# Optimization experiments

Hardware: AMD Instinct MI355X
Metric: run time of the kernel (lower is better)

## Reference

```python
import jax, jax.numpy as jnp
import numpy as np

B, S, D, F, H, E = 2, 1024, 1024, 4096, 16, 8
EPS = 1e-5


def _layernorm(x, w, b):
    m = jnp.mean(x, -1, keepdims=True)
    v = jnp.var(x, -1, keepdims=True)
    return (x - m) * jax.lax.rsqrt(v + EPS) * w + b


def _rope(x):
    # rotary embedding applied over full embed dim (split-half convention)
    b, s, d = x.shape
    half = d // 2
    inv = 1.0 / (10000.0 ** (jnp.arange(half, dtype=jnp.float32) / half))
    ang = jnp.arange(s, dtype=jnp.float32)[:, None] * inv[None, :]  # [S, half]
    cos, sin = jnp.cos(ang), jnp.sin(ang)
    x1, x2 = x[..., :half], x[..., half:]
    return jnp.concatenate([x1 * cos - x2 * sin, x1 * sin + x2 * cos], -1)


def setup_inputs() -> dict:
    key = jax.random.key(0)
    ks = jax.random.split(key, 9)
    sc = 0.02
    return {
        "x": jax.random.normal(ks[0], (B, S, D), jnp.float32),
        "ln1_w": jnp.ones((D,), jnp.float32),
        "ln1_b": jnp.zeros((D,), jnp.float32),
        "ln2_w": jnp.ones((D,), jnp.float32),
        "ln2_b": jnp.zeros((D,), jnp.float32),
        "w_qkv": jax.random.normal(ks[1], (3 * D, D), jnp.float32) * sc,
        "b_qkv": jnp.zeros((3 * D,), jnp.float32),
        "w_out": jax.random.normal(ks[2], (D, D), jnp.float32) * sc,
        "b_out": jnp.zeros((D,), jnp.float32),
        "w_router": jax.random.normal(ks[3], (D, E), jnp.float32) * sc,
        "wi": jax.random.normal(ks[4], (E, D, F), jnp.float32) * sc,  # per-expert wi (no bias)
        "wo": jax.random.normal(ks[5], (E, F // 2, D), jnp.float32) * sc,  # swiglu halves ffn dim
    }


def reference(x, ln1_w, ln1_b, ln2_w, ln2_b, w_qkv, b_qkv, w_out, b_out, w_router, wi, wo):
    # ---- pre-norm self-attention block ----
    residual = x
    h = _layernorm(x, ln1_w, ln1_b)
    h = _rope(h)
    qkv = h @ w_qkv.T + b_qkv  # [B,S,3D]
    q, k, v = jnp.split(qkv, 3, axis=-1)
    hd = D // H
    to_heads = lambda t: t.reshape(B, S, H, hd).transpose(0, 2, 1, 3)
    q, k, v = to_heads(q), to_heads(k), to_heads(v)
    scale = 1.0 / np.sqrt(hd).astype(np.float32)
    att = jax.nn.softmax(jnp.einsum('bhqd,bhkd->bhqk', q, k) * scale, axis=-1)
    o = jnp.einsum('bhqk,bhkd->bhqd', att, v).transpose(0, 2, 1, 3).reshape(B, S, D)
    o = o @ w_out.T + b_out
    x = residual + o  # attn dropout is identity at eval

    # ---- pre-norm sparse MoE FFN block ----
    residual = x
    h = _layernorm(x, ln2_w, ln2_b)
    # top-1 router in float32
    logits = h.astype(jnp.float32) @ w_router  # [B,S,E]
    probs = jax.nn.softmax(logits, axis=-1)
    mask = jax.nn.one_hot(jnp.argmax(probs, -1), E, dtype=h.dtype)  # expert_mask
    gate = probs.astype(h.dtype) * mask  # router_probs * expert_mask, [B,S,E]
    # dense all-expert compute, masked combine (same math as gather/scatter loop)
    hid = jnp.einsum('bsd,edf->bsef', h, wi)  # [B,S,E,F]
    a, g = jnp.split(hid, 2, axis=-1)
    act = jax.nn.silu(a) * g  # SwiGLU, [B,S,E,F/2]
    y = jnp.einsum('bsef,efd,bse->bsd', act, wo, gate)
    x = residual + y
    return x, logits
```

## Files before the change

### kernel.cpp

```cpp
#include <hip/hip_runtime.h>
#include <hip/hip_bf16.h>
#include <math.h>

#define BB 2
#define SS 1024
#define DD 1024
#define FF 4096
#define HH 16
#define EE 8
#define MM (BB*SS)
#define MAX_TILES 24
#define MAX_TILES2 40

typedef __attribute__((ext_vector_type(8))) short bf16x8;
typedef __attribute__((ext_vector_type(8))) short s16x8;
typedef __attribute__((ext_vector_type(4))) float f32x4;

#define OFF_WIT  ((size_t)0)
#define OFF_WOT  ((size_t)67108864)
#define OFF_WQH  ((size_t)100663296)
#define OFF_WQL  ((size_t)106954752)
#define OFF_WOH  ((size_t)113246208)
#define OFF_WOL  ((size_t)115343360)
#define OFF_H1H  ((size_t)117440512)
#define OFF_H1L  ((size_t)121634816)
#define OFF_QKV  ((size_t)125829120)
#define OFF_OH   ((size_t)150994944)
#define OFF_OL   ((size_t)155189248)
#define OFF_X2   ((size_t)159383552)
#define OFF_H2B  ((size_t)167772160)
#define OFF_ACT  ((size_t)171966464)
#define OFF_GATE ((size_t)180879360)
#define OFF_EID  ((size_t)180887552)
#define OFF_PERM ((size_t)180895744)
#define OFF_CNT  ((size_t)180903936)
#define OFF_FILL ((size_t)180903968)
#define OFF_NT   ((size_t)180904000)
#define OFF_TE   ((size_t)180904192)
#define OFF_TS   ((size_t)180904320)
#define OFF_TR   ((size_t)180904448)
#define OFF_TE2  ((size_t)180904576)
#define OFF_TS2  ((size_t)180904768)
#define OFF_TR2  ((size_t)180904960)
#define OFF_NT2  ((size_t)180905152)
#define OFF_KSH  OFF_WQH
#define OFF_KSL  (OFF_WQH + 4194304)
#define OFF_VTH  OFF_H1H
#define OFF_VTL  OFF_H1L

__device__ __forceinline__ void gload16(const void* g, void* l) {
    __builtin_amdgcn_global_load_lds(
        (const __attribute__((address_space(1))) unsigned int*)g,
        (__attribute__((address_space(3))) unsigned int*)l, 16, 0, 0);
}

__device__ __forceinline__ short bfh(float v) {
    __hip_bfloat16 h = __float2bfloat16(v);
    return *(short*)&h;
}
__device__ __forceinline__ float bf2f(short s) {
    __hip_bfloat16 h = *(__hip_bfloat16*)&s;
    return __bfloat162float(h);
}

__device__ __forceinline__ void split_write(float v, __hip_bfloat16* hp, __hip_bfloat16* lp, size_t idx) {
    __hip_bfloat16 h = __float2bfloat16(v);
    hp[idx] = h;
    lp[idx] = __float2bfloat16(v - __bfloat162float(h));
}

__device__ __forceinline__ void tcvt64_body(const float* __restrict__ in, __hip_bfloat16* __restrict__ out,
                                            int R, int C, int r0, int c0, float* tile , int t) {
    {
        int ri = t >> 2, cj = (t & 3) * 16;
        const float* ip = &in[(size_t)(r0 + ri) * C + c0 + cj];
#pragma unroll
        for (int k = 0; k < 4; ++k) {
            float4 v = *(const float4*)(ip + k * 4);
            tile[ri * 65 + cj + k * 4 + 0] = v.x;
            tile[ri * 65 + cj + k * 4 + 1] = v.y;
            tile[ri * 65 + cj + k * 4 + 2] = v.z;
            tile[ri * 65 + cj + k * 4 + 3] = v.w;
        }
    }
    __syncthreads();
    {
        int co = t >> 2, rj = (t & 3) * 16;
        bf16x8 v8a, v8b;
#pragma unroll
        for (int q = 0; q < 8; ++q) v8a[q] = bfh(tile[(rj + q) * 65 + co]);
#pragma unroll
        for (int q = 0; q < 8; ++q) v8b[q] = bfh(tile[(rj + 8 + q) * 65 + co]);
        __hip_bfloat16* op = &out[(size_t)(c0 + co) * R + r0 + rj];
        *(bf16x8*)op = v8a;
        *(bf16x8*)(op + 8) = v8b;
    }
}

__global__ void k_phase0(const float* __restrict__ x, const float* __restrict__ ln1w,
                         const float* __restrict__ ln1b,
                         __hip_bfloat16* __restrict__ h1H, __hip_bfloat16* __restrict__ h1L,
                         const float* __restrict__ w_qkv, __hip_bfloat16* __restrict__ wqH,
                         __hip_bfloat16* __restrict__ wqL,
                         const float* __restrict__ w_out, __hip_bfloat16* __restrict__ woH,
                         __hip_bfloat16* __restrict__ woL) {
    __shared__ __align__(16) float smem[1032];
    int bid = blockIdx.x, t = threadIdx.x;
    if (bid < 2048) {
        int m = bid, s = m & (SS - 1);
        float* row = smem;
        float* red = smem + 1024;
        const float* xp = x + (size_t)m * DD;
        float sum = 0.f, sumsq = 0.f;
#pragma unroll
        for (int l = 0; l < 4; ++l) {
            int i = t + l * 256;
            float v = xp[i];
            row[i] = v;
            sum += v; sumsq += v * v;
        }
#pragma unroll
        for (int off = 32; off; off >>= 1) {
            sum   += __shfl_xor(sum, off);
            sumsq += __shfl_xor(sumsq, off);
        }
        int wid = t >> 6, lane = t & 63;
        if (lane == 0) { red[wid] = sum; red[4 + wid] = sumsq; }
        __syncthreads();
        sum   = red[0] + red[1] + red[2] + red[3];
        sumsq = red[4] + red[5] + red[6] + red[7];
        float mean = sum * (1.f / DD);
        float var  = sumsq * (1.f / DD) - mean * mean;
        float rstd = rsqrtf(var + 1e-5f);
        size_t base = (size_t)m * DD;
        const float kln = logf(10000.f) / 512.f;
#pragma unroll
        for (int l = 0; l < 2; ++l) {
            int i = t + l * 256;
            float n1 = (row[i]       - mean) * rstd * ln1w[i]       + ln1b[i];
            float n2 = (row[i + 512] - mean) * rstd * ln1w[i + 512] + ln1b[i + 512];
            float inv = expf(-(float)i * kln);
            float ang = (float)s * inv;
            float c = cosf(ang), sn = sinf(ang);
            split_write(n1 * c - n2 * sn,  h1H, h1L, base + i);
            split_write(n1 * sn + n2 * c, h1H, h1L, base + i + 512);
        }
    } else if (bid < 5120) {
        int idx = (bid - 2048) * 256 + t;
        float4 v = ((const float4*)w_qkv)[idx];
        split_write(v.x, wqH, wqL, (size_t)idx * 4 + 0);
        split_write(v.y, wqH, wqL, (size_t)idx * 4 + 1);
        split_write(v.z, wqH, wqL, (size_t)idx * 4 + 2);
        split_write(v.w, wqH, wqL, (size_t)idx * 4 + 3);
    } else {
        int idx = (bid - 5120) * 256 + t;
        float4 v = ((const float4*)w_out)[idx];
        split_write(v.x, woH, woL, (size_t)idx * 4 + 0);
        split_write(v.y, woH, woL, (size_t)idx * 4 + 1);
        split_write(v.z, woH, woL, (size_t)idx * 4 + 2);
        split_write(v.w, woH, woL, (size_t)idx * 4 + 3);
    }
}

__global__ void k_qkv(const __hip_bfloat16* __restrict__ Ah, const __hip_bfloat16* __restrict__ Al,
                      const __hip_bfloat16* __restrict__ Bh, const __hip_bfloat16* __restrict__ Bl,
                      const float* __restrict__ bias, float* __restrict__ Cf) {
    __shared__ __align__(16) short AsH[64 * 32];
    __shared__ __align__(16) short AsL[64 * 32];
    __shared__ __align__(16) short BsH[128 * 32];
    __shared__ __align__(16) short BsL[128 * 32];
    const int N = 3072, K = DD;
    int bid = blockIdx.x;
    int xcd = bid & 7, idx = bid >> 3;
    int nt = xcd + (idx >> 5) * 8;
    int mt = idx & 31;
    int m0 = mt * 64, n0 = nt * 128;
    const int t = threadIdx.x;
    const int w = t >> 6, lane = t & 63;
    const int sid = w * 64 + lane;
    const int g = lane >> 4, r16 = lane & 15;

    f32x4 acc[4][2] = {};

    for (int k0 = 0; k0 < K; k0 += 32) {
        {
            int rrow = sid >> 2, sl = sid & 3;
            int slog = sl ^ ((rrow >> 1) & 3);
            size_t lbase = (size_t)(w * 64) * 8;
            size_t gaoff = (size_t)(m0 + rrow) * K + k0 + slog * 8;
            gload16(Ah + gaoff, &AsH[lbase]);
            gload16(Al + gaoff, &AsL[lbase]);
        }
#pragma unroll
        for (int j = 0; j < 2; ++j) {
            int id = j * 256 + sid;
            int rrow = id >> 2, sl = id & 3;
            int slog = sl ^ ((rrow >> 1) & 3);
            size_t lbase = (size_t)(j * 256 + w * 64) * 8;
            size_t gboff = (size_t)(n0 + rrow) * K + k0 + slog * 8;
            gload16(Bh + gboff, &BsH[lbase]);
            gload16(Bl + gboff, &BsL[lbase]);
        }
        __syncthreads();
        bf16x8 ah[4], al[4], bh[2], bl[2];
#pragma unroll
        for (int i = 0; i < 4; ++i) {
            int ra = i * 16 + r16;
            int pa = g ^ ((ra >> 1) & 3);
            ah[i] = *(const bf16x8*)&AsH[ra * 32 + pa * 8];
            al[i] = *(const bf16x8*)&AsL[ra * 32 + pa * 8];
        }
#pragma unroll
        for (int n = 0; n < 2; ++n) {
            int rb = w * 32 + n * 16 + r16;
            int pb = g ^ ((rb >> 1) & 3);
            bh[n] = *(const bf16x8*)&BsH[rb * 32 + pb * 8];
            bl[n] = *(const bf16x8*)&BsL[rb * 32 + pb * 8];
        }
#pragma unroll
        for (int i = 0; i < 4; ++i)
#pragma unroll
            for (int n = 0; n < 2; ++n) {
                acc[i][n] = __builtin_amdgcn_mfma_f32_16x16x32_bf16(ah[i], bh[n], acc[i][n], 0, 0, 0);
                acc[i][n] = __builtin_amdgcn_mfma_f32_16x16x32_bf16(ah[i], bl[n], acc[i][n], 0, 0, 0);
                acc[i][n] = __builtin_amdgcn_mfma_f32_16x16x32_bf16(al[i], bh[n], acc[i][n], 0, 0, 0);
            }
        __syncthreads();
    }

#pragma unroll
    for (int i = 0; i < 4; ++i) {
#pragma unroll
        for (int n = 0; n < 2; ++n) {
            int col = n0 + w * 32 + n * 16 + r16;
#pragma unroll
            for (int q = 0; q < 4; ++q) {
                int r = m0 + i * 16 + g * 4 + q;
                Cf[(size_t)r * N + col] = acc[i][n][q] + bias[col];
            }
        }
    }
}

__global__ void k_oproj64(const __hip_bfloat16* __restrict__ Ah, const __hip_bfloat16* __restrict__ Al,
                          const __hip_bfloat16* __restrict__ Bh, const __hip_bfloat16* __restrict__ Bl,
                          const float* __restrict__ bias, const float* __restrict__ addsrc,
                          float* __restrict__ Cf, int* __restrict__ zero17) {
    __shared__ __align__(16) short AsH[64 * 32];
    __shared__ __align__(16) short AsL[64 * 32];
    __shared__ __align__(16) short BsH[128 * 32];
    __shared__ __align__(16) short BsL[128 * 32];
    const int N = DD, K = DD;
    int bid = blockIdx.x;
    int m0 = (bid >> 3) * 64, n0 = (bid & 7) * 128;
    const int t = threadIdx.x;
    if (bid == 0 && t < 17) zero17[t] = 0;
    const int w = t >> 6, lane = t & 63;
    const int sid = w * 64 + lane;
    const int g = lane >> 4, r16 = lane & 15;

    f32x4 acc[4][2] = {};

    for (int k0 = 0; k0 < K; k0 += 32) {
        {
            int rrow = sid >> 2, sl = sid & 3;
            int slog = sl ^ ((rrow >> 1) & 3);
            size_t lbase = (size_t)(w * 64) * 8;
            size_t gaoff = (size_t)(m0 + rrow) * K + k0 + slog * 8;
            gload16(Ah + gaoff, &AsH[lbase]);
            gload16(Al + gaoff, &AsL[lbase]);
        }
#pragma unroll
        for (int j = 0; j < 2; ++j) {
            int id = j * 256 + sid;
            int rrow = id >> 2, sl = id & 3;
            int slog = sl ^ ((rrow >> 1) & 3);
            size_t lbase = (size_t)(j * 256 + w * 64) * 8;
            size_t gboff = (size_t)(n0 + rrow) * K + k0 + slog * 8;
            gload16(Bh + gboff, &BsH[lbase]);
            gload16(Bl + gboff, &BsL[lbase]);
        }
        __syncthreads();
        bf16x8 ah[4], al[4], bh[2], bl[2];
#pragma unroll
        for (int i = 0; i < 4; ++i) {
            int ra = i * 16 + r16;
            int pa = g ^ ((ra >> 1) & 3);
            ah[i] = *(const bf16x8*)&AsH[ra * 32 + pa * 8];
            al[i] = *(const bf16x8*)&AsL[ra * 32 + pa * 8];
        }
#pragma unroll
        for (int n = 0; n < 2; ++n) {
            int rb = w * 32 + n * 16 + r16;
            int pb = g ^ ((rb >> 1) & 3);
            bh[n] = *(const bf16x8*)&BsH[rb * 32 + pb * 8];
            bl[n] = *(const bf16x8*)&BsL[rb * 32 + pb * 8];
        }
#pragma unroll
        for (int i = 0; i < 4; ++i)
#pragma unroll
            for (int n = 0; n < 2; ++n) {
                acc[i][n] = __builtin_amdgcn_mfma_f32_16x16x32_bf16(ah[i], bh[n], acc[i][n], 0, 0, 0);
                acc[i][n] = __builtin_amdgcn_mfma_f32_16x16x32_bf16(ah[i], bl[n], acc[i][n], 0, 0, 0);
                acc[i][n] = __builtin_amdgcn_mfma_f32_16x16x32_bf16(al[i], bh[n], acc[i][n], 0, 0, 0);
            }
        __syncthreads();
    }

#pragma unroll
    for (int i = 0; i < 4; ++i) {
#pragma unroll
        for (int n = 0; n < 2; ++n) {
            int col = n0 + w * 32 + n * 16 + r16;
#pragma unroll
            for (int q = 0; q < 4; ++q) {
                int r = m0 + i * 16 + g * 4 + q;
                Cf[(size_t)r * N + col] =
                    acc[i][n][q] + bias[col] + addsrc[(size_t)r * N + col];
            }
        }
    }
}

__global__ void k_moe_up(const __hip_bfloat16* __restrict__ A,
                         const __hip_bfloat16* __restrict__ Bt,
                         __hip_bfloat16* __restrict__ act,
                         const int* __restrict__ perm,
                         const int* __restrict__ te, const int* __restrict__ ts,
                         const int* __restrict__ tr, const int* __restrict__ ntl) {
    __shared__ __align__(16) short As[128 * 32];
    __shared__ __align__(16) short Bs[128 * 32];
    __shared__ int permS[128];
    int tile = blockIdx.y;
    if (tile >= *ntl) return;
    int e = te[tile], rs = ts[tile], rows = tr[tile];
    const int t = threadIdx.x;
    if (t < 128) permS[t] = (t < rows) ? perm[rs + t] : 0;
    __syncthreads();
    int c0 = blockIdx.x * 64;
    const int w = t >> 6, lane = t & 63;
    const int wr = w >> 1, wc = w & 1;
    const int sid = w * 64 + lane;
    const int g = lane >> 4, r16 = lane & 15;

    const __hip_bfloat16* Bp = Bt + (size_t)e * FF * DD;

    f32x4 acc[4][4] = {};

    for (int k0 = 0; k0 < DD; k0 += 32) {
#pragma unroll
        for (int j = 0; j < 2; ++j) {
            int id = j * 256 + sid;
            int rrow = id >> 2, sl = id & 3;
            int slog = sl ^ ((rrow >> 1) & 3);
            size_t lbase = (size_t)(j * 256 + w * 64) * 8;
            gload16(A + (size_t)permS[rrow] * DD + k0 + slog * 8, &As[lbase]);
            int q = rrow >> 4, rr = rrow & 15;
            int wrow = c0 + (q >> 2) * 32 + ((q & 3) >> 1) * 16 + rr + (q & 1) * 2048;
            gload16(Bp + (size_t)wrow * DD + k0 + slog * 8, &Bs[lbase]);
        }
        __syncthreads();
        bf16x8 af[4], bfr[4];
#pragma unroll
        for (int i = 0; i < 4; ++i) {
            int ra = wr * 64 + i * 16 + r16;
            int pa = g ^ ((ra >> 1) & 3);
            af[i] = *(const bf16x8*)&As[ra * 32 + pa * 8];
            int rb = wc * 64 + i * 16 + r16;
            int pb = g ^ ((rb >> 1) & 3);
            bfr[i] = *(const bf16x8*)&Bs[rb * 32 + pb * 8];
        }
#pragma unroll
        for (int i = 0; i < 4; ++i)
#pragma unroll
            for (int n = 0; n < 4; ++n)
                acc[i][n] = __builtin_amdgcn_mfma_f32_16x16x32_bf16(af[i], bfr[n], acc[i][n], 0, 0, 0);
        __syncthreads();
    }

#pragma unroll
    for (int i = 0; i < 4; ++i) {
#pragma unroll
        for (int p2 = 0; p2 < 2; ++p2) {
            int col = c0 + wc * 32 + p2 * 16 + r16;
#pragma unroll
            for (int q = 0; q < 4; ++q) {
                int r = wr * 64 + i * 16 + g * 4 + q;
                if (r < rows) {
                    float a  = acc[i][2 * p2][q];
                    float gv = acc[i][2 * p2 + 1][q];
                    act[(size_t)(rs + r) * 2048 + col] =
                        __float2bfloat16((a / (1.f + expf(-a))) * gv);
                }
            }
        }
    }
}

__global__ void k_moe_dn(const __hip_bfloat16* __restrict__ A,
                         const __hip_bfloat16* __restrict__ Bt,
                         const float* __restrict__ addsrc, float* __restrict__ Cf,
                         const int* __restrict__ perm,
                         const int* __restrict__ te2, const int* __restrict__ ts2,
                         const int* __restrict__ tr2, const int* __restrict__ ntl2,
                         const float* __restrict__ gate) {
    __shared__ __align__(16) short As[64 * 32];
    __shared__ __align__(16) short Bs[128 * 32];
    __shared__ int permS[64];
    int tile = blockIdx.y;
    if (tile >= *ntl2) return;
    int e = te2[tile], rs = ts2[tile], rows = tr2[tile];
    const int t = threadIdx.x;
    if (t < 64) permS[t] = (t < rows) ? perm[rs + t] : 0;
    __syncthreads();
    int n0 = blockIdx.x * 128;
    const int w = t >> 6, lane = t & 63;
    const int sid = w * 64 + lane;
    const int g = lane >> 4, r16 = lane & 15;
    const int K = FF / 2;

    const __hip_bfloat16* Bp = Bt + (size_t)e * DD * (FF / 2);

    f32x4 acc[4][2] = {};

    for (int k0 = 0; k0 < K; k0 += 32) {
        {
            int rrow = sid >> 2, sl = sid & 3;
            int slog = sl ^ ((rrow >> 1) & 3);
            size_t lbase = (size_t)(w * 64) * 8;
            gload16(A + (size_t)(rs + rrow) * K + k0 + slog * 8, &As[lbase]);
        }
#pragma unroll
        for (int j = 0; j < 2; ++j) {
            int id = j * 256 + sid;
            int rrow = id >> 2, sl = id & 3;
            int slog = sl ^ ((rrow >> 1) & 3);
            size_t lbase = (size_t)(j * 256 + w * 64) * 8;
            gload16(Bp + (size_t)(n0 + rrow) * K + k0 + slog * 8, &Bs[lbase]);
        }
        __syncthreads();
        bf16x8 af[4], bfr[2];
#pragma unroll
        for (int i = 0; i < 4; ++i) {
            int ra = i * 16 + r16;
            int pa = g ^ ((ra >> 1) & 3);
            af[i] = *(const bf16x8*)&As[ra * 32 + pa * 8];
        }
#pragma unroll
        for (int n = 0; n < 2; ++n) {
            int rb = w * 32 + n * 16 + r16;
            int pb = g ^ ((rb >> 1) & 3);
            bfr[n] = *(const bf16x8*)&Bs[rb * 32 + pb * 8];
        }
#pragma unroll
        for (int i = 0; i < 4; ++i)
#pragma unroll
            for (int n = 0; n < 2; ++n)
                acc[i][n] = __builtin_amdgcn_mfma_f32_16x16x32_bf16(af[i], bfr[n], acc[i][n], 0, 0, 0);
        __syncthreads();
    }

#pragma unroll
    for (int i = 0; i < 4; ++i) {
#pragma unroll
        for (int n = 0; n < 2; ++n) {
            int col = n0 + w * 32 + n * 16 + r16;
#pragma unroll
            for (int q = 0; q < 4; ++q) {
                int r = i * 16 + g * 4 + q;
                if (r >= rows) continue;
                int tok = permS[r];
                Cf[(size_t)tok * DD + col] = addsrc[(size_t)tok * DD + col] + gate[tok] * acc[i][n][q];
            }
        }
    }
}

__global__ void k_prep(const float* __restrict__ qkv, short* __restrict__ KH, short* __restrict__ KL,
                       short* __restrict__ VH, short* __restrict__ VL) {
    __shared__ float tile[64][65];
    int b = blockIdx.z, h = blockIdx.y, s0 = blockIdx.x * 64;
    int t = threadIdx.x;
    int row = t >> 2, c0 = (t & 3) * 16;
    const float* kp = qkv + (size_t)(b * SS + s0 + row) * 3072 + 1024 + h * 64 + c0;
    const float* vp = kp + 1024;
    {
        size_t krow = ((size_t)(b * HH + h) * SS + s0 + row) * 64;
        int key = (s0 + row) & 7;
#pragma unroll
        for (int g2 = 0; g2 < 2; ++g2) {
            s16x8 hv, lv;
#pragma unroll
            for (int j = 0; j < 8; ++j) {
                float v = kp[g2 * 8 + j];
                short hh = bfh(v);
                hv[j] = hh; lv[j] = bfh(v - bf2f(hh));
            }
            int p = ((c0 >> 3) + g2) ^ key;
            *(s16x8*)&KH[krow + p * 8] = hv;
            *(s16x8*)&KL[krow + p * 8] = lv;
        }
    }
#pragma unroll
    for (int j = 0; j < 16; ++j) tile[row][c0 + j] = vp[j];
    __syncthreads();
    {
        int d = t >> 2, sc = (t & 3) * 16;
        size_t vrow = ((size_t)(b * HH + h) * 64 + d) * SS + s0;
        int key = d & 7;
#pragma unroll
        for (int g2 = 0; g2 < 2; ++g2) {
            s16x8 hv, lv;
#pragma unroll
            for (int j = 0; j < 8; ++j) {
                float v = tile[sc + g2 * 8 + j][d];
                short hh = bfh(v);
                hv[j] = hh; lv[j] = bfh(v - bf2f(hh));
            }
            int p = ((sc >> 3) + g2) ^ key;
            *(s16x8*)&VH[vrow + p * 8] = hv;
            *(s16x8*)&VL[vrow + p * 8] = lv;
        }
    }
}

#define LDP 72
__global__ __launch_bounds__(512, 4)
void k_attn_mega(const float* __restrict__ qkv,
                 const short* __restrict__ KH, const short* __restrict__ KL,
                 const short* __restrict__ VH, const short* __restrict__ VL,
                 __hip_bfloat16* __restrict__ ohi, __hip_bfloat16* __restrict__ olo,
                 const float* __restrict__ wi, __hip_bfloat16* __restrict__ wiT,
                 const float* __restrict__ wo, __hip_bfloat16* __restrict__ woT) {
    __shared__ __align__(16) char smem[69632];
    int id = blockIdx.x;
    if (id >= 256) {
        int t512 = threadIdx.x;
        int half = t512 >> 8, t = t512 & 255;
        float* tile = (float*)(smem + half * 33280 / 2 * 2);
        tile = (float*)(smem + half * 16640);
        if (id < 4352) {
            int gidx = (id - 256) * 2 + half;
            int e = gidx >> 10, rem = gidx & 1023;
            int ry = rem >> 6, cx = rem & 63;
            tcvt64_body(wi + (size_t)e * DD * FF, wiT + (size_t)e * DD * FF,
                        1024, 4096, ry * 64, cx * 64, tile, t);
        } else {
            int gidx = (id - 4352) * 2 + half;
            int e = gidx >> 9, rem = gidx & 511;
            int ry = rem >> 4, cx = rem & 15;
            tcvt64_body(wo + (size_t)e * 2048 * 1024, woT + (size_t)e * 2048 * 1024,
                        2048, 1024, ry * 64, cx * 64, tile, t);
        }
        return;
    }
    short* Ks  = (short*)smem;
    short* Kl2 = (short*)(smem + 8192);
    short* Vs  = (short*)(smem + 16384);
    short* Vl2 = (short*)(smem + 24576);
    int xcd = id & 7, slot = id >> 3;
    int bh = xcd * 4 + (slot >> 3);
    int q0 = (slot & 7) * 128;
    int b = bh >> 4, h = bh & 15;
    int t = threadIdx.x;
    int w = t >> 6, lane = t & 63;
    int g = lane >> 4, r16 = lane & 15;
    int srow = t >> 3, sslot = t & 7;
    short* PhS = (short*)(smem + 32768 + w * 2304);
    short* PlS = (short*)(smem + 51200 + w * 2304);

    const size_t kbase = ((size_t)bh * SS) * 64;
    const size_t vbase = ((size_t)bh * 64) * SS;

    bf16x8 qfh[2], qfl[2];
    {
        const float* qp = qkv + (size_t)(b * SS + q0 + w * 16 + r16) * 3072 + h * 64;
#pragma unroll
        for (int ks = 0; ks < 2; ++ks) {
            float vv[8];
            *(float4*)&vv[0] = *(const float4*)(qp + ks * 32 + g * 8);
            *(float4*)&vv[4] = *(const float4*)(qp + ks * 32 + g * 8 + 4);
#pragma unroll
            for (int j = 0; j < 8; ++j) {
                float sv = vv[j] * 0.125f;
                short hh = bfh(sv);
                qfh[ks][j] = hh;
                qfl[ks][j] = bfh(sv - bf2f(hh));
            }
        }
    }

    float mrun[4], lrun[4];
    f32x4 oacc[4] = {};
#pragma unroll
    for (int q = 0; q < 4; ++q) { mrun[q] = -1e30f; lrun[q] = 0.f; }

    for (int k0 = 0; k0 < SS; k0 += 64) {
        gload16(KH + kbase + (size_t)(k0 + srow) * 64 + sslot * 8, Ks  + w * 512);
        gload16(KL + kbase + (size_t)(k0 + srow) * 64 + sslot * 8, Kl2 + w * 512);
        gload16(VH + vbase + (size_t)srow * SS + k0 + sslot * 8,   Vs  + w * 512);
        gload16(VL + vbase + (size_t)srow * SS + k0 + sslot * 8,   Vl2 + w * 512);
        __syncthreads();

        f32x4 accs[4] = {};
#pragma unroll
        for (int ks = 0; ks < 2; ++ks) {
            bf16x8 kfh[4], kfl[4];
#pragma unroll
            for (int n = 0; n < 4; ++n) {
                int rb = n * 16 + r16;
                int p = (ks * 4 + g) ^ (r16 & 7);
                kfh[n] = *(const bf16x8*)&Ks[rb * 64 + p * 8];
                kfl[n] = *(const bf16x8*)&Kl2[rb * 64 + p * 8];
            }
            __builtin_amdgcn_s_setprio(1);
#pragma unroll
            for (int n = 0; n < 4; ++n) {
                accs[n] = __builtin_amdgcn_mfma_f32_16x16x32_bf16(qfh[ks], kfh[n], accs[n], 0, 0, 0);
                accs[n] = __builtin_amdgcn_mfma_f32_16x16x32_bf16(qfh[ks], kfl[n], accs[n], 0, 0, 0);
                accs[n] = __builtin_amdgcn_mfma_f32_16x16x32_bf16(qfl[ks], kfh[n], accs[n], 0, 0, 0);
            }
            __builtin_amdgcn_s_setprio(0);
        }

        float mn[4], corr[4], psum[4];
#pragma unroll
        for (int q = 0; q < 4; ++q) {
            float m = fmaxf(fmaxf(accs[0][q], accs[1][q]), fmaxf(accs[2][q], accs[3][q]));
            m = fmaxf(m, __shfl_xor(m, 1));
            m = fmaxf(m, __shfl_xor(m, 2));
            m = fmaxf(m, __shfl_xor(m, 4));
            m = fmaxf(m, __shfl_xor(m, 8));
            mn[q] = fmaxf(mrun[q], m);
            corr[q] = expf(mrun[q] - mn[q]);
            mrun[q] = mn[q];
            psum[q] = 0.f;
        }
#pragma unroll
        for (int n = 0; n < 4; ++n)
#pragma unroll
            for (int q = 0; q < 4; ++q) {
                float p = expf(accs[n][q] - mn[q]);
                psum[q] += p;
                short ph = bfh(p);
                PhS[(g * 4 + q) * LDP + n * 16 + r16] = ph;
                PlS[(g * 4 + q) * LDP + n * 16 + r16] = bfh(p - bf2f(ph));
            }
#pragma unroll
        for (int q = 0; q < 4; ++q) {
            psum[q] += __shfl_xor(psum[q], 1);
            psum[q] += __shfl_xor(psum[q], 2);
            psum[q] += __shfl_xor(psum[q], 4);
            psum[q] += __shfl_xor(psum[q], 8);
            lrun[q] = lrun[q] * corr[q] + psum[q];
#pragma unroll
            for (int n = 0; n < 4; ++n) oacc[n][q] *= corr[q];
        }

#pragma unroll
        for (int ks = 0; ks < 2; ++ks) {
            bf16x8 vfh[4], vfl[4];
#pragma unroll
            for (int n = 0; n < 4; ++n) {
                int rb = n * 16 + r16;
                int p = (ks * 4 + g) ^ (r16 & 7);
                vfh[n] = *(const bf16x8*)&Vs[rb * 64 + p * 8];
                vfl[n] = *(const bf16x8*)&Vl2[rb * 64 + p * 8];
            }
            bf16x8 pfh = *(const bf16x8*)&PhS[r16 * LDP + ks * 32 + g * 8];
            bf16x8 pfl = *(const bf16x8*)&PlS[r16 * LDP + ks * 32 + g * 8];
            __builtin_amdgcn_s_setprio(1);
#pragma unroll
            for (int n = 0; n < 4; ++n) {
                oacc[n] = __builtin_amdgcn_mfma_f32_16x16x32_bf16(pfh, vfh[n], oacc[n], 0, 0, 0);
                oacc[n] = __builtin_amdgcn_mfma_f32_16x16x32_bf16(pfh, vfl[n], oacc[n], 0, 0, 0);
                oacc[n] = __builtin_amdgcn_mfma_f32_16x16x32_bf16(pfl, vfh[n], oacc[n], 0, 0, 0);
            }
            __builtin_amdgcn_s_setprio(0);
        }
        __syncthreads();
    }

    float invl[4];
#pragma unroll
    for (int q = 0; q < 4; ++q) invl[q] = 1.f / lrun[q];
#pragma unroll
    for (int n = 0; n < 4; ++n) {
        int col = h * 64 + n * 16 + r16;
#pragma unroll
        for (int q = 0; q < 4; ++q) {
            int rowg = b * SS + q0 + w * 16 + g * 4 + q;
            split_write(oacc[n][q] * invl[q], ohi, olo, (size_t)rowg * DD + col);
        }
    }
}

__global__ void k_ln2_router(const float* __restrict__ x2, const float* __restrict__ w,
                             const float* __restrict__ b, const float* __restrict__ wr,
                             __hip_bfloat16* __restrict__ h2b, float* __restrict__ logits,
                             float* __restrict__ gate, int* __restrict__ eid,
                             int* __restrict__ counts) {
    int m = blockIdx.x, t = threadIdx.x;
    __shared__ float red[8];
    __shared__ float racc[4][8];
    const float* xp = x2 + (size_t)m * DD;
    float v[4];
    float sum = 0.f, sumsq = 0.f;
#pragma unroll
    for (int l = 0; l < 4; ++l) {
        v[l] = xp[t + l * 256];
        sum += v[l]; sumsq += v[l] * v[l];
    }
#pragma unroll
    for (int off = 32; off; off >>= 1) {
        sum   += __shfl_xor(sum, off);
        sumsq += __shfl_xor(sumsq, off);
    }
    int wid = t >> 6, lane = t & 63;
    if (lane == 0) { red[wid] = sum; red[4 + wid] = sumsq; }
    __syncthreads();
    sum   = red[0] + red[1] + red[2] + red[3];
    sumsq = red[4] + red[5] + red[6] + red[7];
    float mean = sum * (1.f / DD);
    float var  = sumsq * (1.f / DD) - mean * mean;
    float rstd = rsqrtf(var + 1e-5f);
    float acc[EE] = {};
#pragma unroll
    for (int l = 0; l < 4; ++l) {
        int i = t + l * 256;
        float hv = (v[l] - mean) * rstd * w[i] + b[i];
        h2b[(size_t)m * DD + i] = __float2bfloat16(hv);
        const float* wp = wr + (size_t)i * EE;
#pragma unroll
        for (int n = 0; n < EE; ++n) acc[n] += hv * wp[n];
    }
#pragma unroll
    for (int off = 32; off; off >>= 1)
#pragma unroll
        for (int n = 0; n < EE; ++n) acc[n] += __shfl_xor(acc[n], off);
    if (lane == 0)
#pragma unroll
        for (int n = 0; n < EE; ++n) racc[wid][n] = acc[n];
    __syncthreads();
    if (t == 0) {
        float lg[EE];
#pragma unroll
        for (int n = 0; n < EE; ++n) lg[n] = racc[0][n] + racc[1][n] + racc[2][n] + racc[3][n];
        float mx = lg[0]; int best = 0;
#pragma unroll
        for (int n = 1; n < EE; ++n) if (lg[n] > mx) { mx = lg[n]; best = n; }
        float den = 0.f;
#pragma unroll
        for (int n = 0; n < EE; ++n) den += expf(lg[n] - mx);
        gate[m] = 1.f / den;
        eid[m] = best;
        atomicAdd(&counts[best], 1);
#pragma unroll
        for (int n = 0; n < EE; ++n) logits[(size_t)m * EE + n] = lg[n];
    }
}

__global__ void k_offscatter(const int* __restrict__ counts,
                             int* __restrict__ te, int* __restrict__ ts, int* __restrict__ tr,
                             int* __restrict__ ntl,
                             int* __restrict__ te2, int* __restrict__ ts2, int* __restrict__ tr2,
                             int* __restrict__ ntl2,
                             const int* __restrict__ eid,
                             int* __restrict__ fill, int* __restrict__ perm) {
    __shared__ int soffs[EE];
    int t = threadIdx.x;
    if (t == 0) {
        int off = 0, nt = 0, nt2 = 0;
        for (int e = 0; e < EE; ++e) {
            soffs[e] = off;
            int c = counts[e];
            for (int t0 = 0; t0 < c; t0 += 128) {
                te[nt] = e; ts[nt] = off + t0; tr[nt] = (c - t0 < 128) ? (c - t0) : 128; ++nt;
            }
            for (int t0 = 0; t0 < c; t0 += 64) {
                te2[nt2] = e; ts2[nt2] = off + t0; tr2[nt2] = (c - t0 < 64) ? (c - t0) : 64; ++nt2;
            }
            off += c;
        }
        *ntl = nt;
        *ntl2 = nt2;
    }
    __syncthreads();
#pragma unroll
    for (int tok = t; tok < MM; tok += 1024) {
        int e = eid[tok];
        int pos = soffs[e] + atomicAdd(&fill[e], 1);
        perm[pos] = tok;
    }
}

extern "C" void kernel_launch(void* const* d_in, const int* in_sizes, int n_in,
                              void* d_out, int out_size, void* d_ws, size_t ws_size,
                              hipStream_t stream) {
    const float* x     = (const float*)d_in[0];
    const float* ln1w  = (const float*)d_in[1];
    const float* ln1b  = (const float*)d_in[2];
    const float* ln2w  = (const float*)d_in[3];
    const float* ln2b  = (const float*)d_in[4];
    const float* w_qkv = (const float*)d_in[5];
    const float* b_qkv = (const float*)d_in[6];
    const float* w_out = (const float*)d_in[7];
    const float* b_out = (const float*)d_in[8];
    const float* w_rtr = (const float*)d_in[9];
    const float* wi    = (const float*)d_in[10];
    const float* wo    = (const float*)d_in[11];
    float* out = (float*)d_out;

    char* wsb = (char*)d_ws;
    __hip_bfloat16* wiT  = (__hip_bfloat16*)(wsb + OFF_WIT);
    __hip_bfloat16* woT  = (__hip_bfloat16*)(wsb + OFF_WOT);
    __hip_bfloat16* wqH  = (__hip_bfloat16*)(wsb + OFF_WQH);
    __hip_bfloat16* wqL  = (__hip_bfloat16*)(wsb + OFF_WQL);
    __hip_bfloat16* woH  = (__hip_bfloat16*)(wsb + OFF_WOH);
    __hip_bfloat16* woL  = (__hip_bfloat16*)(wsb + OFF_WOL);
    __hip_bfloat16* h1H  = (__hip_bfloat16*)(wsb + OFF_H1H);
    __hip_bfloat16* h1L  = (__hip_bfloat16*)(wsb + OFF_H1L);
    float*          qkvF = (float*)(wsb + OFF_QKV);
    __hip_bfloat16* oH   = (__hip_bfloat16*)(wsb + OFF_OH);
    __hip_bfloat16* oL   = (__hip_bfloat16*)(wsb + OFF_OL);
    float*          x2F  = (float*)(wsb + OFF_X2);
    __hip_bfloat16* h2B  = (__hip_bfloat16*)(wsb + OFF_H2B);
    __hip_bfloat16* actB = (__hip_bfloat16*)(wsb + OFF_ACT);
    short* KSH = (short*)(wsb + OFF_KSH);
    short* KSL = (short*)(wsb + OFF_KSL);
    short* VTH = (short*)(wsb + OFF_VTH);
    short* VTL = (short*)(wsb + OFF_VTL);
    float* gate = (float*)(wsb + OFF_GATE);
    int* eid    = (int*)(wsb + OFF_EID);
    int* perm   = (int*)(wsb + OFF_PERM);
    int* counts = (int*)(wsb + OFF_CNT);
    int* fill   = (int*)(wsb + OFF_FILL);
    int* ntl    = (int*)(wsb + OFF_NT);
    int* te     = (int*)(wsb + OFF_TE);
    int* tsx    = (int*)(wsb + OFF_TS);
    int* trx    = (int*)(wsb + OFF_TR);
    int* te2    = (int*)(wsb + OFF_TE2);
    int* ts2    = (int*)(wsb + OFF_TS2);
    int* tr2    = (int*)(wsb + OFF_TR2);
    int* ntl2   = (int*)(wsb + OFF_NT2);

    k_phase0<<<6144, 256, 0, stream>>>(x, ln1w, ln1b, h1H, h1L, w_qkv, wqH, wqL,
                                       w_out, woH, woL);
    k_qkv<<<768, 256, 0, stream>>>(h1H, h1L, wqH, wqL, b_qkv, qkvF);
    k_prep<<<dim3(SS / 64, HH, BB), 256, 0, stream>>>(qkvF, KSH, KSL, VTH, VTL);
    k_attn_mega<<<6400, 512, 0, stream>>>(qkvF, KSH, KSL, VTH, VTL, oH, oL,
                                          wi, wiT, wo, woT);
    k_oproj64<<<256, 256, 0, stream>>>(oH, oL, woH, woL, b_out, x, x2F, counts);
    k_ln2_router<<<MM, 256, 0, stream>>>(x2F, ln2w, ln2b, w_rtr, h2B,
                                         out + (size_t)MM * DD, gate, eid, counts);
    k_offscatter<<<1, 1024, 0, stream>>>(counts, te, tsx, trx, ntl,
                                         te2, ts2, tr2, ntl2, eid, fill, perm);
    k_moe_up<<<dim3(32, MAX_TILES), 256, 0, stream>>>(h2B, wiT, actB, perm, te, tsx, trx, ntl);
    k_moe_dn<<<dim3(DD / 128, MAX_TILES2), 256, 0, stream>>>(
        actB, woT, x2F, out, perm, te2, ts2, tr2, ntl2, gate);
}
```

Measured before the change: 307.0 us.

## Read fp32 expert weights directly in MoE GEMMs and double-buffer attention KV

Removes the bulk pre-transposition of the expert weights into bf16 that ran inside the attention launch as extra blocks. The MoE up and down kernels now load fp32 weight tiles straight from wi/wo, convert them to bf16 in registers and scatter them into swizzled shared memory. This avoids writing and re-reading a full bf16 weight copy, at the cost of touching only weights for the experts actually used. The attention kernel becomes a standalone 256-block launch with double-buffered K/V tiles, so the next tile's loads overlap compute. Risks include uncoalesced scalar LDS writes, bank conflicts during the on-the-fly transpose, and fp32 loads that carry twice the bytes of bf16.

```diff
diff --git a/kernel.cpp b/kernel.cpp
--- a/kernel.cpp
+++ b/kernel.cpp
@@ -16,8 +16,6 @@
 typedef __attribute__((ext_vector_type(8))) short s16x8;
 typedef __attribute__((ext_vector_type(4))) float f32x4;
 
-#define OFF_WIT  ((size_t)0)
-#define OFF_WOT  ((size_t)67108864)
 #define OFF_WQH  ((size_t)100663296)
 #define OFF_WQL  ((size_t)106954752)
 #define OFF_WOH  ((size_t)113246208)
@@ -69,34 +67,6 @@
     lp[idx] = __float2bfloat16(v - __bfloat162float(h));
 }
 
-__device__ __forceinline__ void tcvt64_body(const float* __restrict__ in, __hip_bfloat16* __restrict__ out,
-                                            int R, int C, int r0, int c0, float* tile , int t) {
-    {
-        int ri = t >> 2, cj = (t & 3) * 16;
-        const float* ip = &in[(size_t)(r0 + ri) * C + c0 + cj];
-#pragma unroll
-        for (int k = 0; k < 4; ++k) {
-            float4 v = *(const float4*)(ip + k * 4);
-            tile[ri * 65 + cj + k * 4 + 0] = v.x;
-            tile[ri * 65 + cj + k * 4 + 1] = v.y;
-            tile[ri * 65 + cj + k * 4 + 2] = v.z;
-            tile[ri * 65 + cj + k * 4 + 3] = v.w;
-        }
-    }
-    __syncthreads();
-    {
-        int co = t >> 2, rj = (t & 3) * 16;
-        bf16x8 v8a, v8b;
-#pragma unroll
-        for (int q = 0; q < 8; ++q) v8a[q] = bfh(tile[(rj + q) * 65 + co]);
-#pragma unroll
-        for (int q = 0; q < 8; ++q) v8b[q] = bfh(tile[(rj + 8 + q) * 65 + co]);
-        __hip_bfloat16* op = &out[(size_t)(c0 + co) * R + r0 + rj];
-        *(bf16x8*)op = v8a;
-        *(bf16x8*)(op + 8) = v8b;
-    }
-}
-
 __global__ void k_phase0(const float* __restrict__ x, const float* __restrict__ ln1w,
                          const float* __restrict__ ln1b,
                          __hip_bfloat16* __restrict__ h1H, __hip_bfloat16* __restrict__ h1L,
@@ -323,7 +293,7 @@
 }
 
 __global__ void k_moe_up(const __hip_bfloat16* __restrict__ A,
-                         const __hip_bfloat16* __restrict__ Bt,
+                         const float* __restrict__ wi,
                          __hip_bfloat16* __restrict__ act,
                          const int* __restrict__ perm,
                          const int* __restrict__ te, const int* __restrict__ ts,
@@ -343,7 +313,13 @@
     const int sid = w * 64 + lane;
     const int g = lane >> 4, r16 = lane & 15;
 
-    const __hip_bfloat16* Bp = Bt + (size_t)e * FF * DD;
+    const float* Bp = wi + (size_t)e * DD * FF;
+
+    const int kk = t >> 3, rem = t & 7;
+    const int T = rem >> 2, Lb = (rem & 3) << 4;
+    const int qidx = (Lb >> 5) * 4 + ((Lb >> 4) & 1) * 2 + T;
+    const int rbb = qidx * 16;
+    const int s8 = kk >> 3, ko = kk & 7;
 
     f32x4 acc[4][4] = {};
 
@@ -355,9 +331,20 @@
             int slog = sl ^ ((rrow >> 1) & 3);
             size_t lbase = (size_t)(j * 256 + w * 64) * 8;
             gload16(A + (size_t)permS[rrow] * DD + k0 + slog * 8, &As[lbase]);
-            int q = rrow >> 4, rr = rrow & 15;
-            int wrow = c0 + (q >> 2) * 32 + ((q & 3) >> 1) * 16 + rr + (q & 1) * 2048;
-            gload16(Bp + (size_t)wrow * DD + k0 + slog * 8, &Bs[lbase]);
+        }
+        {
+            const float* wp = Bp + (size_t)(k0 + kk) * FF + c0 + T * 2048 + Lb;
+            float vv[16];
+            *(float4*)&vv[0]  = *(const float4*)(wp);
+            *(float4*)&vv[4]  = *(const float4*)(wp + 4);
+            *(float4*)&vv[8]  = *(const float4*)(wp + 8);
+            *(float4*)&vv[12] = *(const float4*)(wp + 12);
+#pragma unroll
+            for (int j = 0; j < 16; ++j) {
+                int rb = rbb + j;
+                int pc = ((s8 ^ ((rb >> 1) & 3)) << 3) | ko;
+                Bs[rb * 32 + pc] = bfh(vv[j]);
+            }
         }
         __syncthreads();
         bf16x8 af[4], bfr[4];
@@ -398,7 +385,7 @@
 }
 
 __global__ void k_moe_dn(const __hip_bfloat16* __restrict__ A,
-                         const __hip_bfloat16* __restrict__ Bt,
+                         const float* __restrict__ wo,
                          const float* __restrict__ addsrc, float* __restrict__ Cf,
                          const int* __restrict__ perm,
                          const int* __restrict__ te2, const int* __restrict__ ts2,
@@ -419,7 +406,11 @@
     const int g = lane >> 4, r16 = lane & 15;
     const int K = FF / 2;
 
-    const __hip_bfloat16* Bp = Bt + (size_t)e * DD * (FF / 2);
+    const float* Bp = wo + (size_t)e * (size_t)K * DD;
+
+    const int kk = t >> 3, rem = t & 7;
+    const int Lb = rem << 4;
+    const int s8 = kk >> 3, ko = kk & 7;
 
     f32x4 acc[4][2] = {};
 
@@ -430,13 +421,19 @@
             size_t lbase = (size_t)(w * 64) * 8;
             gload16(A + (size_t)(rs + rrow) * K + k0 + slog * 8, &As[lbase]);
         }
-#pragma unroll
-        for (int j = 0; j < 2; ++j) {
-            int id = j * 256 + sid;
-            int rrow = id >> 2, sl = id & 3;
-            int slog = sl ^ ((rrow >> 1) & 3);
-            size_t lbase = (size_t)(j * 256 + w * 64) * 8;
-            gload16(Bp + (size_t)(n0 + rrow) * K + k0 + slog * 8, &Bs[lbase]);
+        {
+            const float* wp = Bp + (size_t)(k0 + kk) * DD + n0 + Lb;
+            float vv[16];
+            *(float4*)&vv[0]  = *(const float4*)(wp);
+            *(float4*)&vv[4]  = *(const float4*)(wp + 4);
+            *(float4*)&vv[8]  = *(const float4*)(wp + 8);
+            *(float4*)&vv[12] = *(const float4*)(wp + 12);
+#pragma unroll
+            for (int j = 0; j < 16; ++j) {
+                int rb = Lb + j;
+                int pc = ((s8 ^ ((rb >> 1) & 3)) << 3) | ko;
+                Bs[rb * 32 + pc] = bfh(vv[j]);
+            }
         }
         __syncthreads();
         bf16x8 af[4], bfr[2];
@@ -525,39 +522,14 @@
 }
 
 #define LDP 72
-__global__ __launch_bounds__(512, 4)
-void k_attn_mega(const float* __restrict__ qkv,
+__global__ __launch_bounds__(512, 1)
+void k_attn_mfma(const float* __restrict__ qkv,
                  const short* __restrict__ KH, const short* __restrict__ KL,
                  const short* __restrict__ VH, const short* __restrict__ VL,
-                 __hip_bfloat16* __restrict__ ohi, __hip_bfloat16* __restrict__ olo,
-                 const float* __restrict__ wi, __hip_bfloat16* __restrict__ wiT,
-                 const float* __restrict__ wo, __hip_bfloat16* __restrict__ woT) {
-    __shared__ __align__(16) char smem[69632];
+                 __hip_bfloat16* __restrict__ ohi, __hip_bfloat16* __restrict__ olo) {
+    __shared__ __align__(16) short Ks[2][64 * 64], Kl2[2][64 * 64], Vs[2][64 * 64], Vl2[2][64 * 64];
+    __shared__ __align__(16) short PhS[8][16 * LDP], PlS[8][16 * LDP];
     int id = blockIdx.x;
-    if (id >= 256) {
-        int t512 = threadIdx.x;
-        int half = t512 >> 8, t = t512 & 255;
-        float* tile = (float*)(smem + half * 33280 / 2 * 2);
-        tile = (float*)(smem + half * 16640);
-        if (id < 4352) {
-            int gidx = (id - 256) * 2 + half;
-            int e = gidx >> 10, rem = gidx & 1023;
-            int ry = rem >> 6, cx = rem & 63;
-            tcvt64_body(wi + (size_t)e * DD * FF, wiT + (size_t)e * DD * FF,
-                        1024, 4096, ry * 64, cx * 64, tile, t);
-        } else {
-            int gidx = (id - 4352) * 2 + half;
-            int e = gidx >> 9, rem = gidx & 511;
-            int ry = rem >> 4, cx = rem & 15;
-            tcvt64_body(wo + (size_t)e * 2048 * 1024, woT + (size_t)e * 2048 * 1024,
-                        2048, 1024, ry * 64, cx * 64, tile, t);
-        }
-        return;
-    }
-    short* Ks  = (short*)smem;
-    short* Kl2 = (short*)(smem + 8192);
-    short* Vs  = (short*)(smem + 16384);
-    short* Vl2 = (short*)(smem + 24576);
     int xcd = id & 7, slot = id >> 3;
     int bh = xcd * 4 + (slot >> 3);
     int q0 = (slot & 7) * 128;
@@ -566,8 +538,6 @@
     int w = t >> 6, lane = t & 63;
     int g = lane >> 4, r16 = lane & 15;
     int srow = t >> 3, sslot = t & 7;
-    short* PhS = (short*)(smem + 32768 + w * 2304);
-    short* PlS = (short*)(smem + 51200 + w * 2304);
 
     const size_t kbase = ((size_t)bh * SS) * 64;
     const size_t vbase = ((size_t)bh * 64) * SS;
@@ -595,12 +565,21 @@
 #pragma unroll
     for (int q = 0; q < 4; ++q) { mrun[q] = -1e30f; lrun[q] = 0.f; }
 
+    gload16(KH + kbase + (size_t)srow * 64 + sslot * 8, &Ks[0][w * 512]);
+    gload16(KL + kbase + (size_t)srow * 64 + sslot * 8, &Kl2[0][w * 512]);
+    gload16(VH + vbase + (size_t)srow * SS + sslot * 8, &Vs[0][w * 512]);
+    gload16(VL + vbase + (size_t)srow * SS + sslot * 8, &Vl2[0][w * 512]);
+    __syncthreads();
+
+    int cur = 0;
     for (int k0 = 0; k0 < SS; k0 += 64) {
-        gload16(KH + kbase + (size_t)(k0 + srow) * 64 + sslot * 8, Ks  + w * 512);
-        gload16(KL + kbase + (size_t)(k0 + srow) * 64 + sslot * 8, Kl2 + w * 512);
-        gload16(VH + vbase + (size_t)srow * SS + k0 + sslot * 8,   Vs  + w * 512);
-        gload16(VL + vbase + (size_t)srow * SS + k0 + sslot * 8,   Vl2 + w * 512);
-        __syncthreads();
+        if (k0 + 64 < SS) {
+            int kn = k0 + 64;
+            gload16(KH + kbase + (size_t)(kn + srow) * 64 + sslot * 8, &Ks[cur ^ 1][w * 512]);
+            gload16(KL + kbase + (size_t)(kn + srow) * 64 + sslot * 8, &Kl2[cur ^ 1][w * 512]);
+            gload16(VH + vbase + (size_t)srow * SS + kn + sslot * 8,   &Vs[cur ^ 1][w * 512]);
+            gload16(VL + vbase + (size_t)srow * SS + kn + sslot * 8,   &Vl2[cur ^ 1][w * 512]);
+        }
 
         f32x4 accs[4] = {};
 #pragma unroll
@@ -610,8 +589,8 @@
             for (int n = 0; n < 4; ++n) {
                 int rb = n * 16 + r16;
                 int p = (ks * 4 + g) ^ (r16 & 7);
-                kfh[n] = *(const bf16x8*)&Ks[rb * 64 + p * 8];
-                kfl[n] = *(const bf16x8*)&Kl2[rb * 64 + p * 8];
+                kfh[n] = *(const bf16x8*)&Ks[cur][rb * 64 + p * 8];
+                kfl[n] = *(const bf16x8*)&Kl2[cur][rb * 64 + p * 8];
             }
             __builtin_amdgcn_s_setprio(1);
 #pragma unroll
@@ -643,8 +622,8 @@
                 float p = expf(accs[n][q] - mn[q]);
                 psum[q] += p;
                 short ph = bfh(p);
-                PhS[(g * 4 + q) * LDP + n * 16 + r16] = ph;
-                PlS[(g * 4 + q) * LDP + n * 16 + r16] = bfh(p - bf2f(ph));
+                PhS[w][(g * 4 + q) * LDP + n * 16 + r16] = ph;
+                PlS[w][(g * 4 + q) * LDP + n * 16 + r16] = bfh(p - bf2f(ph));
             }
 #pragma unroll
         for (int q = 0; q < 4; ++q) {
@@ -664,11 +643,11 @@
             for (int n = 0; n < 4; ++n) {
                 int rb = n * 16 + r16;
                 int p = (ks * 4 + g) ^ (r16 & 7);
-                vfh[n] = *(const bf16x8*)&Vs[rb * 64 + p * 8];
-                vfl[n] = *(const bf16x8*)&Vl2[rb * 64 + p * 8];
-            }
-            bf16x8 pfh = *(const bf16x8*)&PhS[r16 * LDP + ks * 32 + g * 8];
-            bf16x8 pfl = *(const bf16x8*)&PlS[r16 * LDP + ks * 32 + g * 8];
+                vfh[n] = *(const bf16x8*)&Vs[cur][rb * 64 + p * 8];
+                vfl[n] = *(const bf16x8*)&Vl2[cur][rb * 64 + p * 8];
+            }
+            bf16x8 pfh = *(const bf16x8*)&PhS[w][r16 * LDP + ks * 32 + g * 8];
+            bf16x8 pfl = *(const bf16x8*)&PlS[w][r16 * LDP + ks * 32 + g * 8];
             __builtin_amdgcn_s_setprio(1);
 #pragma unroll
             for (int n = 0; n < 4; ++n) {
@@ -679,6 +658,7 @@
             __builtin_amdgcn_s_setprio(0);
         }
         __syncthreads();
+        cur ^= 1;
     }
 
     float invl[4];
@@ -812,8 +792,6 @@
     float* out = (float*)d_out;
 
     char* wsb = (char*)d_ws;
-    __hip_bfloat16* wiT  = (__hip_bfloat16*)(wsb + OFF_WIT);
-    __hip_bfloat16* woT  = (__hip_bfloat16*)(wsb + OFF_WOT);
     __hip_bfloat16* wqH  = (__hip_bfloat16*)(wsb + OFF_WQH);
     __hip_bfloat16* wqL  = (__hip_bfloat16*)(wsb + OFF_WQL);
     __hip_bfloat16* woH  = (__hip_bfloat16*)(wsb + OFF_WOH);
@@ -848,14 +826,13 @@
                                        w_out, woH, woL);
     k_qkv<<<768, 256, 0, stream>>>(h1H, h1L, wqH, wqL, b_qkv, qkvF);
     k_prep<<<dim3(SS / 64, HH, BB), 256, 0, stream>>>(qkvF, KSH, KSL, VTH, VTL);
-    k_attn_mega<<<6400, 512, 0, stream>>>(qkvF, KSH, KSL, VTH, VTL, oH, oL,
-                                          wi, wiT, wo, woT);
+    k_attn_mfma<<<256, 512, 0, stream>>>(qkvF, KSH, KSL, VTH, VTL, oH, oL);
     k_oproj64<<<256, 256, 0, stream>>>(oH, oL, woH, woL, b_out, x, x2F, counts);
     k_ln2_router<<<MM, 256, 0, stream>>>(x2F, ln2w, ln2b, w_rtr, h2B,
                                          out + (size_t)MM * DD, gate, eid, counts);
     k_offscatter<<<1, 1024, 0, stream>>>(counts, te, tsx, trx, ntl,
                                          te2, ts2, tr2, ntl2, eid, fill, perm);
-    k_moe_up<<<dim3(32, MAX_TILES), 256, 0, stream>>>(h2B, wiT, actB, perm, te, tsx, trx, ntl);
+    k_moe_up<<<dim3(32, MAX_TILES), 256, 0, stream>>>(h2B, wi, actB, perm, te, tsx, trx, ntl);
     k_moe_dn<<<dim3(DD / 128, MAX_TILES2), 256, 0, stream>>>(
-        actB, woT, x2F, out, perm, te2, ts2, tr2, ntl2, gate);
-}
+        actB, wo, x2F, out, perm, te2, ts2, tr2, ntl2, gate);
+}
```

Result: slower. 388.4 us (+26.5%).
